# Performance work log

Hardware: AMD Instinct MI355X
Metric: run time of the kernel (lower is better)

## Reference

```python
import jax, jax.numpy as jnp
import numpy as np

NUM_HEADS = 12
HEAD_DIM = 64  # embed_dim 768 / 12 heads
EMBED_DIM = 768
LN_EPS = 1e-5


def _rope_cos_sin(seq_len, dim, dtype):
    # ESM-style RotaryEmbedding: inv_freq over even indices, emb = cat(freqs, freqs)
    inv_freq = 1.0 / (10000.0 ** (jnp.arange(0, dim, 2, dtype=jnp.float32) / dim))
    t = jnp.arange(seq_len, dtype=jnp.float32)
    freqs = t[:, None] * inv_freq[None, :]          # [S, dim/2]
    emb = jnp.concatenate([freqs, freqs], axis=-1)  # [S, dim]
    return jnp.cos(emb).astype(dtype), jnp.sin(emb).astype(dtype)


def _rotate_half(x):
    x1, x2 = jnp.split(x, 2, axis=-1)
    return jnp.concatenate([-x2, x1], axis=-1)


def _apply_rope(x, cos, sin):
    # x: [B, H, S, D]; cos/sin: [S, D]
    return x * cos[None, None] + _rotate_half(x) * sin[None, None]


def setup_inputs() -> dict:
    key = jax.random.key(0)
    ks = jax.random.split(key, 12)
    B, S = 2, 2048

    def xavier(k, shape):
        fan_out, fan_in = shape
        bound = np.sqrt(6.0 / (fan_in + fan_out))
        return jax.random.uniform(k, shape, jnp.float32, -bound, bound)

    return {
        "s_repre": jax.random.normal(ks[0], (B, S, 128), jnp.float32),
        "plm_repre": jax.random.normal(ks[1], (B, S, 1280), jnp.float32),
        "Wq": xavier(ks[2], (EMBED_DIM, 1280)), "bq": jnp.zeros((EMBED_DIM,), jnp.float32),
        "Wk": xavier(ks[3], (EMBED_DIM, 128)),  "bk": jnp.zeros((EMBED_DIM,), jnp.float32),
        "Wv": xavier(ks[4], (EMBED_DIM, 128)),  "bv": jnp.zeros((EMBED_DIM,), jnp.float32),
        "Wo": xavier(ks[5], (1280, EMBED_DIM)), "bo": jnp.zeros((1280,), jnp.float32),
        "ln_g": jnp.ones((1280,), jnp.float32), "ln_b": jnp.zeros((1280,), jnp.float32),
        "Wd": xavier(ks[6], (640, 1280)), "bd": jnp.zeros((640,), jnp.float32),
        "Wu": xavier(ks[7], (1280, 640)), "bu": jnp.zeros((1280,), jnp.float32),
    }


def _forward(s_repre, plm_repre, Wq, bq, Wk, bk, Wv, bv, Wo, bo, ln_g, ln_b, Wd, bd, Wu, bu):
    B, S, _ = s_repre.shape
    H, D = NUM_HEADS, HEAD_DIM
    # QKV projections (torch Linear: x @ W.T + b)
    q = (plm_repre @ Wq.T + bq).reshape(B, S, H, D).transpose(0, 2, 1, 3)
    k = (s_repre @ Wk.T + bk).reshape(B, S, H, D).transpose(0, 2, 1, 3)
    v = (s_repre @ Wv.T + bv).reshape(B, S, H, D).transpose(0, 2, 1, 3)
    cos, sin = _rope_cos_sin(S, D, q.dtype)
    q = _apply_rope(q, cos, sin)
    k = _apply_rope(k, cos, sin)
    # scaled dot-product attention
    logits = jnp.einsum("bhqd,bhkd->bhqk", q, k) / jnp.sqrt(jnp.asarray(D, q.dtype))
    attention = jax.nn.softmax(logits, axis=-1)
    vals = jnp.einsum("bhqk,bhkd->bhqd", attention, v)
    vals = vals.transpose(0, 2, 1, 3).reshape(B, S, H * D)
    o = vals @ Wo.T + bo
    # residual + LayerNorm
    x = o + plm_repre
    mu = jnp.mean(x, axis=-1, keepdims=True)
    var = jnp.mean(jnp.square(x - mu), axis=-1, keepdims=True)
    x = (x - mu) / jnp.sqrt(var + LN_EPS) * ln_g + ln_b
    residual = x
    # GELU FFN (exact erf GELU, matching nn.GELU default)
    h = jax.nn.gelu(x @ Wd.T + bd, approximate=False)
    out = h @ Wu.T + bu + residual
    return out, attention


def reference(s_repre, plm_repre, Wq, bq, Wk, bk, Wv, bv, Wo, bo, ln_g, ln_b, Wd, bd, Wu, bu):
    return _forward(s_repre, plm_repre, Wq, bq, Wk, bk, Wv, bv, Wo, bo, ln_g, ln_b, Wd, bd, Wu, bu)
```

## Files before the change

kernel.cpp:

```cpp
#include <hip/hip_runtime.h>
#include <hip/hip_bf16.h>
#include <math.h>

#define BATCH 2
#define SEQ   2048
#define NH    12
#define HD    64
#define EMB   768
#define PLM   1280
#define FFN   640
#define MROWS (BATCH*SEQ)

typedef __attribute__((ext_vector_type(8))) short short8;
typedef __attribute__((ext_vector_type(4))) float floatx4;

#define MFMA16(a,b,c) __builtin_amdgcn_mfma_f32_16x16x32_bf16((a),(b),(c),0,0,0)

static __device__ __forceinline__ float b2f(ushort u) {
    return __uint_as_float(((unsigned)u) << 16);
}
static __device__ __forceinline__ ushort f2b(float f) {
    unsigned x = __float_as_uint(f);
    unsigned r = (x + 0x7fffu + ((x >> 16) & 1u)) >> 16;
    return (ushort)r;
}
static __device__ __forceinline__ ushort2 f2b2(float a, float b) {
    __hip_bfloat162 h = __float22bfloat162_rn(make_float2(a, b));
    union { __hip_bfloat162 h2; ushort2 u2; } c; c.h2 = h;
    return c.u2;
}

#define CV0 131072
#define CV1 1441792
#define CV2 1687552
#define CV3 1712128
#define CV4 1736704
#define CV5 1982464
#define CV6 2187264
#define CV7 2392064

__global__ __launch_bounds__(256) void cvt_all(
    const float* __restrict__ s0, const float* __restrict__ s1,
    const float* __restrict__ s2, const float* __restrict__ s3,
    const float* __restrict__ s4, const float* __restrict__ s5,
    const float* __restrict__ s6, const float* __restrict__ s7,
    ushort* __restrict__ dst)
{
    int i = blockIdx.x * 256 + threadIdx.x;
    const float* src; int start;
    if      (i < CV0) { src = s0; start = 0;   }
    else if (i < CV1) { src = s1; start = CV0; }
    else if (i < CV2) { src = s2; start = CV1; }
    else if (i < CV3) { src = s3; start = CV2; }
    else if (i < CV4) { src = s4; start = CV3; }
    else if (i < CV5) { src = s5; start = CV4; }
    else if (i < CV6) { src = s6; start = CV5; }
    else              { src = s7; start = CV6; }
    float4 v = ((const float4*)src)[i - start];
    ushort2 a = f2b2(v.x, v.y), b = f2b2(v.z, v.w);
    ushort4 o; o.x = a.x; o.y = a.y; o.z = b.x; o.w = b.y;
    ((ushort4*)dst)[i] = o;
}

static __device__ __forceinline__ void stage_tile(
    const ushort* __restrict__ g,
    int strideBytes,
    int tid, ushort* lds)
{
    const int l   = tid & 63;
    const int w   = tid >> 6;
    const int sub = l >> 3;
    const int scol = (((l & 7) << 4) ^ (sub << 4));
#pragma unroll
    for (int s = 0; s < 2; ++s) {
        const int row = s * 32 + w * 8 + sub;
        const char* gp = (const char*)g + (size_t)row * strideBytes + scol;
        char* lp = (char*)lds + s * 4096 + w * 1024;
        __builtin_amdgcn_global_load_lds(
            (const __attribute__((address_space(1))) void*)gp,
            (__attribute__((address_space(3))) void*)lp, 16, 0, 0);
    }
}

template<int EPI>
__global__ __launch_bounds__(256, 4) void gemm_nt(
    const ushort* __restrict__ A,
    const ushort* __restrict__ W,
    const float*  __restrict__ bias,
    const float*  __restrict__ residF,
    const ushort* __restrict__ residB,
    void* __restrict__ out_,
    int M, int N, int K)
{
    __shared__ __align__(16) ushort As[2][64 * 64];
    __shared__ __align__(16) ushort Bs[2][64 * 64];

    const int tid  = threadIdx.x;
    const int wave = tid >> 6;
    const int lane = tid & 63;
    const int quad = lane >> 4;
    const int col  = lane & 15;
    const int m0   = blockIdx.x * 64 + wave * 16;
    const int n0   = blockIdx.y * 64;

    const int strideBytes = K * 2;
    const ushort* Ag = A + (size_t)(blockIdx.x * 64) * K;
    const ushort* Wg = W + (size_t)n0 * K;

    const int sw = (col & 7) << 4;
    const int a_off0 = (wave * 16 + col) * 128 + ((quad * 16) ^ sw);
    const int a_off1 = (wave * 16 + col) * 128 + ((64 + quad * 16) ^ sw);
    int b_off[8];
#pragma unroll
    for (int f = 0; f < 4; ++f) {
        int rb = (f * 16 + col) * 128;
        b_off[2 * f]     = rb + ((quad * 16) ^ sw);
        b_off[2 * f + 1] = rb + ((64 + quad * 16) ^ sw);
    }

    const floatx4 zero = {0.f, 0.f, 0.f, 0.f};
    floatx4 acc[4] = {zero, zero, zero, zero};

    stage_tile(Ag, strideBytes, tid, As[0]);
    stage_tile(Wg, strideBytes, tid, Bs[0]);
    __syncthreads();

    int buf = 0;
    for (int k0 = 0; k0 < K; k0 += 64) {
        if (k0 + 64 < K) {
            stage_tile(Ag + (k0 + 64), strideBytes, tid, As[buf ^ 1]);
            stage_tile(Wg + (k0 + 64), strideBytes, tid, Bs[buf ^ 1]);
        }
        const char* Ab = (const char*)&As[buf][0];
        const char* Bb = (const char*)&Bs[buf][0];
        short8 a0 = *(const short8*)(Ab + a_off0);
        short8 a1 = *(const short8*)(Ab + a_off1);
        short8 b[8];
#pragma unroll
        for (int f = 0; f < 8; ++f) b[f] = *(const short8*)(Bb + b_off[f]);
#pragma unroll
        for (int f = 0; f < 4; ++f) {
            acc[f] = MFMA16(a0, b[2 * f], acc[f]);
            acc[f] = MFMA16(a1, b[2 * f + 1], acc[f]);
        }
        __syncthreads();
        buf ^= 1;
    }

    float bs[4];
#pragma unroll
    for (int f = 0; f < 4; ++f) bs[f] = bias[n0 + f * 16 + col];

    if constexpr (EPI == 1) {
        ushort* out = (ushort*)out_;
        const int h = n0 >> 6;
#pragma unroll
        for (int r = 0; r < 4; ++r) {
            int m = m0 + quad * 4 + r;
            int b_ = m >> 11, s = m & (SEQ - 1);
            size_t obase = ((size_t)(b_ * NH + h) * SEQ + s) * HD;
#pragma unroll
            for (int f = 0; f < 2; ++f) {
                int d = f * 16 + col;
                float x1 = acc[f][r] + bs[f];
                float x2 = acc[f + 2][r] + bs[f + 2];
                float invf = __expf((float)d * -0.2878231366242557f);
                float theta = (float)s * invf;
                float sn, cs;
                sincosf(theta, &sn, &cs);
                out[obase + d]      = f2b(x1 * cs - x2 * sn);
                out[obase + d + 32] = f2b(x2 * cs + x1 * sn);
            }
        }
    } else if constexpr (EPI == 2) {
        ushort (*tile)[72] = (ushort (*)[72])&As[0][0];
        ushort* out = (ushort*)out_;
        const int h = n0 >> 6;
        const int mi0 = wave * 16 + quad * 4;
#pragma unroll
        for (int r = 0; r < 4; ++r)
#pragma unroll
            for (int f = 0; f < 4; ++f)
                tile[f * 16 + col][mi0 + r] = f2b(acc[f][r] + bs[f]);
        __syncthreads();
        const int mblk = blockIdx.x * 64;
        const int b_ = mblk >> 11, s0 = mblk & (SEQ - 1);
#pragma unroll
        for (int i = 0; i < 2; ++i) {
            int d = (tid >> 3) + i * 32;
            int c = (tid & 7) * 8;
            short8 v = *(const short8*)&tile[d][c];
            *(short8*)&out[((size_t)((b_ * NH + h) * HD + d)) * SEQ + s0 + c] = v;
        }
    } else if constexpr (EPI == 3) {
        ushort* out = (ushort*)out_;
#pragma unroll
        for (int r = 0; r < 4; ++r) {
            int m = m0 + quad * 4 + r;
#pragma unroll
            for (int f = 0; f < 4; ++f) {
                size_t idx = (size_t)m * N + n0 + f * 16 + col;
                out[idx] = f2b(acc[f][r] + bs[f] + residF[idx]);
            }
        }
    } else if constexpr (EPI == 4) {
        ushort* out = (ushort*)out_;
#pragma unroll
        for (int r = 0; r < 4; ++r) {
            int m = m0 + quad * 4 + r;
#pragma unroll
            for (int f = 0; f < 4; ++f) {
                size_t idx = (size_t)m * N + n0 + f * 16 + col;
                float y = acc[f][r] + bs[f];
                out[idx] = f2b(0.5f * y * (1.0f + erff(y * 0.70710678118654752f)));
            }
        }
    } else {
        float* out = (float*)out_;
#pragma unroll
        for (int r = 0; r < 4; ++r) {
            int m = m0 + quad * 4 + r;
#pragma unroll
            for (int f = 0; f < 4; ++f) {
                size_t idx = (size_t)m * N + n0 + f * 16 + col;
                out[idx] = acc[f][r] + bs[f] + b2f(residB[idx]);
            }
        }
    }
}

#define PSTRIDE 68

__global__ __launch_bounds__(256, 4) void attn_kernel(
    const ushort* __restrict__ qb, const ushort* __restrict__ kb,
    const ushort* __restrict__ vb,
    float* __restrict__ attn_out,
    ushort* __restrict__ vals)
{
    const int qt   = blockIdx.x;
    const int bh   = blockIdx.y;
    const int tid  = threadIdx.x;
    const int wave = tid >> 6;
    const int lane = tid & 63;
    const int quad = lane >> 4;
    const int col  = lane & 15;
    const int kv0  = wave * 512;
    const int qrow0 = qt * 16;

    __shared__ __align__(16) float P32[4][16 * PSTRIDE];
    __shared__ float SS[4][16];

    const floatx4 zero = {0.f, 0.f, 0.f, 0.f};

    const ushort* qrow = qb + ((size_t)bh * SEQ + qrow0 + col) * HD + quad * 8;
    short8 aq0 = *(const short8*)qrow;
    short8 aq1 = *(const short8*)(qrow + 32);

    const ushort* kbase = kb + (size_t)bh * SEQ * HD + (size_t)(kv0 + col) * HD + quad * 8;
    const ushort* vbase = vb + (size_t)bh * HD * SEQ + (size_t)col * SEQ + kv0 + quad * 8;

    float sums[4] = {0.f, 0.f, 0.f, 0.f};
    for (int ch = 0; ch < 8; ++ch) {
#pragma unroll
        for (int f = 0; f < 4; ++f) {
            const ushort* kr = kbase + (size_t)(ch * 64 + f * 16) * HD;
            short8 b0 = *(const short8*)kr;
            short8 b1 = *(const short8*)(kr + 32);
            floatx4 t = MFMA16(aq0, b0, zero);
            t = MFMA16(aq1, b1, t);
#pragma unroll
            for (int r = 0; r < 4; ++r) sums[r] += __expf(t[r] * 0.125f);
        }
    }
#pragma unroll
    for (int r = 0; r < 4; ++r) {
        float v = sums[r];
        v += __shfl_xor(v, 1); v += __shfl_xor(v, 2);
        v += __shfl_xor(v, 4); v += __shfl_xor(v, 8);
        sums[r] = v;
    }
    if (col == 0) {
#pragma unroll
        for (int r = 0; r < 4; ++r) SS[wave][quad * 4 + r] = sums[r];
    }
    __syncthreads();
    float rinv[4];
#pragma unroll
    for (int r = 0; r < 4; ++r) {
        int row = quad * 4 + r;
        rinv[r] = 1.0f / (SS[0][row] + SS[1][row] + SS[2][row] + SS[3][row]);
    }

    const size_t gbase = (size_t)bh * SEQ + qrow0;
    floatx4 acco[4] = {zero, zero, zero, zero};
    for (int ch = 0; ch < 8; ++ch) {
#pragma unroll
        for (int f = 0; f < 4; ++f) {
            const ushort* kr = kbase + (size_t)(ch * 64 + f * 16) * HD;
            short8 b0 = *(const short8*)kr;
            short8 b1 = *(const short8*)(kr + 32);
            floatx4 t = MFMA16(aq0, b0, zero);
            t = MFMA16(aq1, b1, t);
#pragma unroll
            for (int r = 0; r < 4; ++r) {
                float p = __expf(t[r] * 0.125f) * rinv[r];
                P32[wave][(quad * 4 + r) * PSTRIDE + f * 16 + col] = p;
            }
        }
#pragma unroll
        for (int it = 0; it < 4; ++it) {
            int row = it * 4 + quad;
            float4 v = *(const float4*)&P32[wave][row * PSTRIDE + col * 4];
            *(float4*)&attn_out[(gbase + row) * SEQ + kv0 + ch * 64 + col * 4] = v;
        }
        const float* pl = &P32[wave][col * PSTRIDE + quad * 8];
        float4 pa = *(const float4*)pl;
        float4 pb = *(const float4*)(pl + 4);
        float4 pc = *(const float4*)(pl + 32);
        float4 pd = *(const float4*)(pl + 36);
        ushort2 c0 = f2b2(pa.x, pa.y), c1 = f2b2(pa.z, pa.w);
        ushort2 c2 = f2b2(pb.x, pb.y), c3 = f2b2(pb.z, pb.w);
        ushort2 c4 = f2b2(pc.x, pc.y), c5 = f2b2(pc.z, pc.w);
        ushort2 c6 = f2b2(pd.x, pd.y), c7 = f2b2(pd.z, pd.w);
        short8 ap0 = {(short)c0.x, (short)c0.y, (short)c1.x, (short)c1.y,
                      (short)c2.x, (short)c2.y, (short)c3.x, (short)c3.y};
        short8 ap1 = {(short)c4.x, (short)c4.y, (short)c5.x, (short)c5.y,
                      (short)c6.x, (short)c6.y, (short)c7.x, (short)c7.y};
#pragma unroll
        for (int f = 0; f < 4; ++f) {
            const ushort* vr = vbase + (size_t)(f * 16) * SEQ + ch * 64;
            short8 b0 = *(const short8*)vr;
            short8 b1 = *(const short8*)(vr + 32);
            acco[f] = MFMA16(ap0, b0, acco[f]);
            acco[f] = MFMA16(ap1, b1, acco[f]);
        }
    }

    __syncthreads();
#pragma unroll
    for (int f = 0; f < 4; ++f)
#pragma unroll
        for (int r = 0; r < 4; ++r)
            P32[wave][(quad * 4 + r) * PSTRIDE + f * 16 + col] = acco[f][r];
    __syncthreads();

    {
        int row = tid >> 4;
        int d0  = (tid & 15) * 4;
        int off = row * PSTRIDE + d0;
        float4 s0 = *(const float4*)&P32[0][off];
        float4 s1 = *(const float4*)&P32[1][off];
        float4 s2 = *(const float4*)&P32[2][off];
        float4 s3 = *(const float4*)&P32[3][off];
        float4 s;
        s.x = s0.x + s1.x + s2.x + s3.x;
        s.y = s0.y + s1.y + s2.y + s3.y;
        s.z = s0.z + s1.z + s2.z + s3.z;
        s.w = s0.w + s1.w + s2.w + s3.w;
        ushort2 u0 = f2b2(s.x, s.y), u1 = f2b2(s.z, s.w);
        ushort4 o; o.x = u0.x; o.y = u0.y; o.z = u1.x; o.w = u1.y;
        const int b = bh / NH, h = bh - b * NH;
        size_t idx = ((size_t)(b * SEQ + qrow0 + row)) * EMB + h * HD + d0;
        *(ushort4*)&vals[idx] = o;
    }
}

__global__ __launch_bounds__(256) void ln_kernel(
    const ushort* __restrict__ x, const float* __restrict__ g,
    const float* __restrict__ bt, ushort* __restrict__ out)
{
    const int row = blockIdx.x;
    const int tid = threadIdx.x;
    const ushort* xr = x + (size_t)row * PLM;

    float xs[5];
    float s = 0.f, s2 = 0.f;
#pragma unroll
    for (int i = 0; i < 5; ++i) {
        float v = b2f(xr[tid + i * 256]);
        xs[i] = v; s += v; s2 += v * v;
    }
#pragma unroll
    for (int off = 1; off < 64; off <<= 1) {
        s  += __shfl_xor(s,  off);
        s2 += __shfl_xor(s2, off);
    }
    __shared__ float red[8];
    const int wave = tid >> 6, lane = tid & 63;
    if (lane == 0) { red[wave] = s; red[4 + wave] = s2; }
    __syncthreads();
    s  = red[0] + red[1] + red[2] + red[3];
    s2 = red[4] + red[5] + red[6] + red[7];
    float mean = s * (1.0f / PLM);
    float var  = s2 * (1.0f / PLM) - mean * mean;
    float rstd = rsqrtf(var + 1e-5f);

    ushort* orow = out + (size_t)row * PLM;
#pragma unroll
    for (int i = 0; i < 5; ++i) {
        int c = tid + i * 256;
        orow[c] = f2b((xs[i] - mean) * rstd * g[c] + bt[c]);
    }
}

extern "C" void kernel_launch(void* const* d_in, const int* in_sizes, int n_in,
                              void* d_out, int out_size, void* d_ws, size_t ws_size,
                              hipStream_t stream)
{
    const float* s_repre = (const float*)d_in[0];
    const float* plm     = (const float*)d_in[1];
    const float* Wq = (const float*)d_in[2];
    const float* bq = (const float*)d_in[3];
    const float* Wk = (const float*)d_in[4];
    const float* bk = (const float*)d_in[5];
    const float* Wv = (const float*)d_in[6];
    const float* bv = (const float*)d_in[7];
    const float* Wo = (const float*)d_in[8];
    const float* bo = (const float*)d_in[9];
    const float* ln_g = (const float*)d_in[10];
    const float* ln_b = (const float*)d_in[11];
    const float* Wd = (const float*)d_in[12];
    const float* bd = (const float*)d_in[13];
    const float* Wu = (const float*)d_in[14];
    const float* bu = (const float*)d_in[15];

    ushort* ws    = (ushort*)d_ws;
    ushort* q_buf = ws;
    ushort* k_buf = q_buf + (size_t)MROWS * EMB;
    ushort* v_buf = k_buf + (size_t)MROWS * EMB;
    ushort* vals  = v_buf + (size_t)MROWS * EMB;
    ushort* x_buf = vals  + (size_t)MROWS * EMB;
    ushort* resid = x_buf + (size_t)MROWS * PLM;
    ushort* h_buf = resid + (size_t)MROWS * PLM;
    ushort* sr_b  = h_buf + (size_t)MROWS * FFN;
    ushort* plm_b = sr_b  + (size_t)MROWS * 128;
    ushort* Wq_b  = plm_b + (size_t)MROWS * PLM;
    ushort* Wk_b  = Wq_b  + (size_t)EMB * PLM;
    ushort* Wv_b  = Wk_b  + (size_t)EMB * 128;
    ushort* Wo_b  = Wv_b  + (size_t)EMB * 128;
    ushort* Wd_b  = Wo_b  + (size_t)PLM * EMB;
    ushort* Wu_b  = Wd_b  + (size_t)FFN * PLM;

    float* out_main = (float*)d_out;
    float* attn_out = out_main + (size_t)MROWS * PLM;

    dim3 blk(256);

    cvt_all<<<dim3(CV7 / 256), blk, 0, stream>>>(
        s_repre, plm, Wq, Wk, Wv, Wo, Wd, Wu, sr_b);

    gemm_nt<1><<<dim3(MROWS / 64, EMB / 64), blk, 0, stream>>>(
        plm_b, Wq_b, bq, nullptr, nullptr, q_buf, MROWS, EMB, PLM);
    gemm_nt<1><<<dim3(MROWS / 64, EMB / 64), blk, 0, stream>>>(
        sr_b, Wk_b, bk, nullptr, nullptr, k_buf, MROWS, EMB, 128);
    gemm_nt<2><<<dim3(MROWS / 64, EMB / 64), blk, 0, stream>>>(
        sr_b, Wv_b, bv, nullptr, nullptr, v_buf, MROWS, EMB, 128);

    attn_kernel<<<dim3(SEQ / 16, BATCH * NH), blk, 0, stream>>>(
        q_buf, k_buf, v_buf, attn_out, vals);

    gemm_nt<3><<<dim3(MROWS / 64, PLM / 64), blk, 0, stream>>>(
        vals, Wo_b, bo, plm, nullptr, x_buf, MROWS, PLM, EMB);

    ln_kernel<<<dim3(MROWS), blk, 0, stream>>>(x_buf, ln_g, ln_b, resid);

    gemm_nt<4><<<dim3(MROWS / 64, FFN / 64), blk, 0, stream>>>(
        resid, Wd_b, bd, nullptr, nullptr, h_buf, MROWS, FFN, PLM);

    gemm_nt<5><<<dim3(MROWS / 64, PLM / 64), blk, 0, stream>>>(
        h_buf, Wu_b, bu, nullptr, resid, out_main, MROWS, PLM, FFN);
}
```

Before: 781.3 us.

## Single-pass attention: stash bf16 exp scores in LDS, normalize after

Merges the two QK^T passes of the attention kernel into one. Unnormalized exp scores are kept as bf16 in a 16x2048 LDS buffer while P@V accumulates, and the row sums are reduced afterwards. The attention probabilities are then written from LDS after rescaling, and the output accumulator is scaled by the inverse sum. This removes the duplicate QK MFMAs and exp work but uses about 66KB of LDS, which lowers occupancy (launch bounds 4 to 2). The written attention matrix now carries bf16 rounding of the exp values.

Result: faster. 733.6 us (-6.1%).

```diff
diff --git a/kernel.cpp b/kernel.cpp
--- a/kernel.cpp
+++ b/kernel.cpp
@@ -229,9 +229,9 @@
     }
 }
 
-#define PSTRIDE 68
-
-__global__ __launch_bounds__(256, 4) void attn_kernel(
+#define EBS 2056
+
+__global__ __launch_bounds__(256, 2) void attn_kernel(
     const ushort* __restrict__ qb, const ushort* __restrict__ kb,
     const ushort* __restrict__ vb,
     float* __restrict__ attn_out,
@@ -247,8 +247,7 @@
     const int kv0  = wave * 512;
     const int qrow0 = qt * 16;
 
-    __shared__ __align__(16) float P32[4][16 * PSTRIDE];
-    __shared__ float SS[4][16];
+    __shared__ __align__(16) ushort Eb[16 * EBS];
 
     const floatx4 zero = {0.f, 0.f, 0.f, 0.f};
 
@@ -260,7 +259,10 @@
     const ushort* vbase = vb + (size_t)bh * HD * SEQ + (size_t)col * SEQ + kv0 + quad * 8;
 
     float sums[4] = {0.f, 0.f, 0.f, 0.f};
+    floatx4 acco[4] = {zero, zero, zero, zero};
+
     for (int ch = 0; ch < 8; ++ch) {
+        const int kvc = kv0 + ch * 64;
 #pragma unroll
         for (int f = 0; f < 4; ++f) {
             const ushort* kr = kbase + (size_t)(ch * 64 + f * 16) * HD;
@@ -268,64 +270,21 @@
             short8 b1 = *(const short8*)(kr + 32);
             floatx4 t = MFMA16(aq0, b0, zero);
             t = MFMA16(aq1, b1, t);
-#pragma unroll
-            for (int r = 0; r < 4; ++r) sums[r] += __expf(t[r] * 0.125f);
-        }
-    }
-#pragma unroll
-    for (int r = 0; r < 4; ++r) {
-        float v = sums[r];
-        v += __shfl_xor(v, 1); v += __shfl_xor(v, 2);
-        v += __shfl_xor(v, 4); v += __shfl_xor(v, 8);
-        sums[r] = v;
-    }
-    if (col == 0) {
-#pragma unroll
-        for (int r = 0; r < 4; ++r) SS[wave][quad * 4 + r] = sums[r];
-    }
-    __syncthreads();
-    float rinv[4];
-#pragma unroll
-    for (int r = 0; r < 4; ++r) {
-        int row = quad * 4 + r;
-        rinv[r] = 1.0f / (SS[0][row] + SS[1][row] + SS[2][row] + SS[3][row]);
-    }
-
-    const size_t gbase = (size_t)bh * SEQ + qrow0;
-    floatx4 acco[4] = {zero, zero, zero, zero};
-    for (int ch = 0; ch < 8; ++ch) {
-#pragma unroll
-        for (int f = 0; f < 4; ++f) {
-            const ushort* kr = kbase + (size_t)(ch * 64 + f * 16) * HD;
-            short8 b0 = *(const short8*)kr;
-            short8 b1 = *(const short8*)(kr + 32);
-            floatx4 t = MFMA16(aq0, b0, zero);
-            t = MFMA16(aq1, b1, t);
-#pragma unroll
-            for (int r = 0; r < 4; ++r) {
-                float p = __expf(t[r] * 0.125f) * rinv[r];
-                P32[wave][(quad * 4 + r) * PSTRIDE + f * 16 + col] = p;
-            }
-        }
-#pragma unroll
-        for (int it = 0; it < 4; ++it) {
-            int row = it * 4 + quad;
-            float4 v = *(const float4*)&P32[wave][row * PSTRIDE + col * 4];
-            *(float4*)&attn_out[(gbase + row) * SEQ + kv0 + ch * 64 + col * 4] = v;
-        }
-        const float* pl = &P32[wave][col * PSTRIDE + quad * 8];
-        float4 pa = *(const float4*)pl;
-        float4 pb = *(const float4*)(pl + 4);
-        float4 pc = *(const float4*)(pl + 32);
-        float4 pd = *(const float4*)(pl + 36);
-        ushort2 c0 = f2b2(pa.x, pa.y), c1 = f2b2(pa.z, pa.w);
-        ushort2 c2 = f2b2(pb.x, pb.y), c3 = f2b2(pb.z, pb.w);
-        ushort2 c4 = f2b2(pc.x, pc.y), c5 = f2b2(pc.z, pc.w);
-        ushort2 c6 = f2b2(pd.x, pd.y), c7 = f2b2(pd.z, pd.w);
-        short8 ap0 = {(short)c0.x, (short)c0.y, (short)c1.x, (short)c1.y,
-                      (short)c2.x, (short)c2.y, (short)c3.x, (short)c3.y};
-        short8 ap1 = {(short)c4.x, (short)c4.y, (short)c5.x, (short)c5.y,
-                      (short)c6.x, (short)c6.y, (short)c7.x, (short)c7.y};
+            float e0 = __expf(t[0] * 0.125f);
+            float e1 = __expf(t[1] * 0.125f);
+            float e2 = __expf(t[2] * 0.125f);
+            float e3 = __expf(t[3] * 0.125f);
+            sums[0] += e0; sums[1] += e1; sums[2] += e2; sums[3] += e3;
+            ushort2 p01 = f2b2(e0, e1), p23 = f2b2(e2, e3);
+            const int cb = kvc + f * 16 + col;
+            Eb[(quad * 4 + 0) * EBS + cb] = p01.x;
+            Eb[(quad * 4 + 1) * EBS + cb] = p01.y;
+            Eb[(quad * 4 + 2) * EBS + cb] = p23.x;
+            Eb[(quad * 4 + 3) * EBS + cb] = p23.y;
+        }
+        const ushort* pl = &Eb[col * EBS + kvc + quad * 8];
+        short8 ap0 = *(const short8*)pl;
+        short8 ap1 = *(const short8*)(pl + 32);
 #pragma unroll
         for (int f = 0; f < 4; ++f) {
             const ushort* vr = vbase + (size_t)(f * 16) * SEQ + ch * 64;
@@ -336,22 +295,75 @@
         }
     }
 
+#pragma unroll
+    for (int r = 0; r < 4; ++r) {
+        float v = sums[r];
+        v += __shfl_xor(v, 1); v += __shfl_xor(v, 2);
+        v += __shfl_xor(v, 4); v += __shfl_xor(v, 8);
+        sums[r] = v;
+    }
+    if (col == 0) {
+#pragma unroll
+        for (int r = 0; r < 4; ++r)
+            *(float*)((char*)Eb + (quad * 4 + r) * (EBS * 2) + 4096 + wave * 4) = sums[r];
+    }
     __syncthreads();
+
+    const size_t gbase = (size_t)bh * SEQ + qrow0;
+#pragma unroll
+    for (int rr = 0; rr < 4; ++rr) {
+        const int row = wave * 4 + rr;
+        float4 ps = *(const float4*)((char*)Eb + row * (EBS * 2) + 4096);
+        float rinv = 1.0f / (ps.x + ps.y + ps.z + ps.w);
+        float* orow = attn_out + (gbase + row) * SEQ;
+#pragma unroll
+        for (int it = 0; it < 4; ++it) {
+            const ushort* src = &Eb[row * EBS + it * 512 + lane * 8];
+            short8 ev = *(const short8*)src;
+            float4 o0, o1;
+            o0.x = b2f((ushort)ev[0]) * rinv; o0.y = b2f((ushort)ev[1]) * rinv;
+            o0.z = b2f((ushort)ev[2]) * rinv; o0.w = b2f((ushort)ev[3]) * rinv;
+            o1.x = b2f((ushort)ev[4]) * rinv; o1.y = b2f((ushort)ev[5]) * rinv;
+            o1.z = b2f((ushort)ev[6]) * rinv; o1.w = b2f((ushort)ev[7]) * rinv;
+            float* dst = orow + it * 512 + lane * 8;
+            *(float4*)dst = o0;
+            *(float4*)(dst + 4) = o1;
+        }
+    }
+
+    {
+        float4 ps0 = *(const float4*)((char*)Eb + (quad * 4 + 0) * (EBS * 2) + 4096);
+        float4 ps1 = *(const float4*)((char*)Eb + (quad * 4 + 1) * (EBS * 2) + 4096);
+        float4 ps2 = *(const float4*)((char*)Eb + (quad * 4 + 2) * (EBS * 2) + 4096);
+        float4 ps3 = *(const float4*)((char*)Eb + (quad * 4 + 3) * (EBS * 2) + 4096);
+        float ri0 = 1.0f / (ps0.x + ps0.y + ps0.z + ps0.w);
+        float ri1 = 1.0f / (ps1.x + ps1.y + ps1.z + ps1.w);
+        float ri2 = 1.0f / (ps2.x + ps2.y + ps2.z + ps2.w);
+        float ri3 = 1.0f / (ps3.x + ps3.y + ps3.z + ps3.w);
+#pragma unroll
+        for (int f = 0; f < 4; ++f) {
+            acco[f][0] *= ri0; acco[f][1] *= ri1;
+            acco[f][2] *= ri2; acco[f][3] *= ri3;
+        }
+    }
+
+    __syncthreads();
+    float* scr = (float*)Eb;
 #pragma unroll
     for (int f = 0; f < 4; ++f)
 #pragma unroll
         for (int r = 0; r < 4; ++r)
-            P32[wave][(quad * 4 + r) * PSTRIDE + f * 16 + col] = acco[f][r];
+            scr[wave * 16 * 68 + (quad * 4 + r) * 68 + f * 16 + col] = acco[f][r];
     __syncthreads();
 
     {
         int row = tid >> 4;
         int d0  = (tid & 15) * 4;
-        int off = row * PSTRIDE + d0;
-        float4 s0 = *(const float4*)&P32[0][off];
-        float4 s1 = *(const float4*)&P32[1][off];
-        float4 s2 = *(const float4*)&P32[2][off];
-        float4 s3 = *(const float4*)&P32[3][off];
+        int off = row * 68 + d0;
+        float4 s0 = *(const float4*)&scr[0 * 16 * 68 + off];
+        float4 s1 = *(const float4*)&scr[1 * 16 * 68 + off];
+        float4 s2 = *(const float4*)&scr[2 * 16 * 68 + off];
+        float4 s3 = *(const float4*)&scr[3 * 16 * 68 + off];
         float4 s;
         s.x = s0.x + s1.x + s2.x + s3.x;
         s.y = s0.y + s1.y + s2.y + s3.y;
```
